# Kernel optimization log

Measured on AMD Instinct MI355X. Metric: run time of the kernel, lower is better.

Reference implementation:

```python
import jax, jax.numpy as jnp
import numpy as np

NUM_GRAPHS = 256
N_NODES = 100000
N_EDGES = 1200000
NODE_DIM = 64
NUM_LAYERS = 3
R_HID = 128
R_OUT = 32


def setup_inputs() -> dict:
    key = jax.random.key(0)
    ks = jax.random.split(key, 10)
    x = jax.random.normal(ks[0], (N_NODES, NODE_DIM), dtype=jnp.float32)
    src = jax.random.randint(ks[1], (N_EDGES,), 0, N_NODES)
    dst = jax.random.randint(ks[2], (N_EDGES,), 0, N_NODES)
    graph_ids = jnp.sort(jax.random.randint(ks[3], (N_NODES,), 0, NUM_GRAPHS))
    s = 1.0 / np.sqrt(NODE_DIM)
    gin_W = jax.random.normal(ks[4], (NUM_LAYERS, NODE_DIM, NODE_DIM), dtype=jnp.float32) * s
    gin_b = jnp.zeros((NUM_LAYERS, NODE_DIM), dtype=jnp.float32)
    eps = jnp.zeros((NUM_LAYERS,), dtype=jnp.float32)  # learnable GIN epsilon
    in_dim = NODE_DIM * NUM_LAYERS
    r_W1 = jax.random.normal(ks[5], (in_dim, R_HID), dtype=jnp.float32) / np.sqrt(in_dim)
    r_b1 = jnp.zeros((R_HID,), dtype=jnp.float32)
    r_W2 = jax.random.normal(ks[6], (R_HID, R_OUT), dtype=jnp.float32) / np.sqrt(R_HID)
    r_b2 = jnp.zeros((R_OUT,), dtype=jnp.float32)
    return {"x": x, "gin_W": gin_W, "gin_b": gin_b, "eps": eps,
            "r_W1": r_W1, "r_b1": r_b1, "r_W2": r_W2, "r_b2": r_b2,
            "src": src, "dst": dst, "graph_ids": graph_ids}


def reference(x, gin_W, gin_b, eps, r_W1, r_b1, r_W2, r_b2, src, dst, graph_ids):
    n = x.shape[0]
    h = x
    hs = []
    for l in range(NUM_LAYERS):  # fixed small layer loop
        # neighbor sum aggregation: scatter-add messages h[src] into dst
        agg = jax.ops.segment_sum(h[src], dst, num_segments=n)  # [N, D]
        h = jax.nn.relu(((1.0 + eps[l]) * h + agg) @ gin_W[l] + gin_b[l])
        hs.append(h)
    H = jnp.stack(hs, axis=1)  # [N, L, D]
    # dgl.sum_nodes per layer output == ragged segment-sum over graph ids
    g = jax.ops.segment_sum(H, graph_ids, num_segments=NUM_GRAPHS)  # [B, L, D]
    g = g.reshape(NUM_GRAPHS, -1)  # [B, L*D]
    # readout MLP (2 layers)
    out = jax.nn.relu(g @ r_W1 + r_b1) @ r_W2 + r_b2
    return out
```

## Files before the change

kernel.cpp:

```cpp
#include <hip/hip_runtime.h>


#define SPLIT 16
#define NBLK 512
#define BS 512

typedef unsigned short ushort_t;
typedef __bf16 v8bf __attribute__((ext_vector_type(8)));
typedef float v4f __attribute__((ext_vector_type(4)));

__device__ __forceinline__ float h2f_lo(unsigned int v) {
    return (float)__builtin_bit_cast(_Float16, (unsigned short)(v & 0xffffu));
}
__device__ __forceinline__ float h2f_hi(unsigned int v) {
    return (float)__builtin_bit_cast(_Float16, (unsigned short)(v >> 16));
}
__device__ __forceinline__ unsigned int f2h(float f) {
    return (unsigned int)__builtin_bit_cast(unsigned short, (_Float16)f);
}

__global__ __launch_bounds__(256) void pre_kernel(
        const int* __restrict__ dst, int* __restrict__ cnt2d,
        int E, int nbkt, int ebpb,
        const float* __restrict__ x, ushort_t* __restrict__ xh, int n4, int castBlocks,
        const float* __restrict__ W, ushort_t* __restrict__ whi,
        ushort_t* __restrict__ wlo, int wtotal) {
    __shared__ int lcnt[256];
    int t = threadIdx.x;
    int blk = blockIdx.x;
    if (blk < NBLK) {
        lcnt[t] = 0;
        __syncthreads();
        int base = blk * ebpb;
        int end = min(base + ebpb, E);
        for (int i = base + t; i < end; i += 256)
            atomicAdd(&lcnt[dst[i] >> 9], 1);
        __syncthreads();
        if (t < nbkt) cnt2d[(size_t)blk * nbkt + t] = lcnt[t];
    } else if (blk < NBLK + castBlocks) {
        int i = (blk - NBLK) * 256 + t;
        if (i < n4) {
            float4 v = ((const float4*)x)[i];
            uint2 p;
            p.x = f2h(v.x) | (f2h(v.y) << 16);
            p.y = f2h(v.z) | (f2h(v.w) << 16);
            ((uint2*)xh)[i] = p;
        }
    } else {
        int i = (blk - NBLK - castBlocks) * 256 + t;
        if (i < wtotal) {
            int l = i >> 12, r = i & 4095;
            int n = r >> 6, k = r & 63;
            float w = W[l * 4096 + k * 64 + n];
            __bf16 h = (__bf16)w;
            float rem = w - (float)h;
            whi[i] = __builtin_bit_cast(ushort_t, h);
            wlo[i] = __builtin_bit_cast(ushort_t, (__bf16)rem);
        }
    }
}

__global__ __launch_bounds__(256) void colscan_kernel(
        const int* __restrict__ cnt2d, int* __restrict__ blkoff,
        int* __restrict__ btot, int nbkt) {
    __shared__ int sh[256];
    int b = blockIdx.x, t = threadIdx.x;
    int i0 = 2 * t, i1 = 2 * t + 1;
    int v0 = cnt2d[(size_t)i0 * nbkt + b];
    int v1 = cnt2d[(size_t)i1 * nbkt + b];
    int pair = v0 + v1;
    sh[t] = pair;
    __syncthreads();
    for (int off = 1; off < 256; off <<= 1) {
        int u = (t >= off) ? sh[t - off] : 0;
        __syncthreads();
        sh[t] += u;
        __syncthreads();
    }
    int ex = sh[t] - pair;
    blkoff[(size_t)b * NBLK + i0] = ex;
    blkoff[(size_t)b * NBLK + i1] = ex + v0;
    if (t == 255) btot[b] = sh[255];
}

__global__ __launch_bounds__(256) void bucket_base_kernel(
        const int* __restrict__ btot, int* __restrict__ bbase,
        int* __restrict__ offsets, int nbkt, int N, int E) {
    __shared__ int sh[256];
    int t = threadIdx.x;
    int v = (t < nbkt) ? btot[t] : 0;
    sh[t] = v;
    __syncthreads();
    for (int off = 1; off < 256; off <<= 1) {
        int u = (t >= off) ? sh[t - off] : 0;
        __syncthreads();
        sh[t] += u;
        __syncthreads();
    }
    if (t < nbkt) bbase[t] = sh[t] - v;
    if (t == 0) { bbase[nbkt] = E; offsets[N] = E; }
}

__global__ __launch_bounds__(256) void bucket_scatter_kernel(
        const int* __restrict__ src, const int* __restrict__ dst,
        const int* __restrict__ bbase, const int* __restrict__ blkoff,
        unsigned int* __restrict__ bkt, int E, int nbkt, int ebpb) {
    __shared__ int lbase[256];
    __shared__ int lrank[256];
    int t = threadIdx.x;
    if (t < nbkt) lbase[t] = bbase[t] + blkoff[(size_t)t * NBLK + blockIdx.x];
    lrank[t] = 0;
    __syncthreads();
    int base = blockIdx.x * ebpb;
    int end = min(base + ebpb, E);
    for (int i = base + t; i < end; i += 256) {
        int d = dst[i];
        int b = d >> 9;
        int r = atomicAdd(&lrank[b], 1);
        bkt[lbase[b] + r] = ((unsigned int)src[i] << 9) | (unsigned int)(d & (BS - 1));
    }
}

__global__ __launch_bounds__(256) void csr_build_kernel(
        const unsigned int* __restrict__ bkt, const int* __restrict__ bbase,
        int* __restrict__ offsets, int* __restrict__ csr, int N, int nbkt) {
    __shared__ int cnt[BS];
    __shared__ int rank[BS];
    __shared__ int sh[256];
    int b = blockIdx.x, t = threadIdx.x;
    cnt[t] = 0; cnt[t + 256] = 0;
    rank[t] = 0; rank[t + 256] = 0;
    __syncthreads();
    int base = bbase[b], end = bbase[b + 1];
    for (int i = base + t; i < end; i += 256)
        atomicAdd(&cnt[bkt[i] & (BS - 1)], 1);
    __syncthreads();
    int i0 = 2 * t, i1 = 2 * t + 1;
    int v0 = cnt[i0], v1 = cnt[i1];
    int pair = v0 + v1;
    sh[t] = pair;
    __syncthreads();
    for (int off = 1; off < 256; off <<= 1) {
        int u = (t >= off) ? sh[t - off] : 0;
        __syncthreads();
        sh[t] += u;
        __syncthreads();
    }
    int ex = sh[t] - pair;
    __syncthreads();
    cnt[i0] = ex;
    cnt[i1] = ex + v0;
    __syncthreads();
    int d0 = (b << 9) + i0;
    if (d0 <= N) offsets[d0] = base + cnt[i0];
    int d1 = (b << 9) + i1;
    if (d1 <= N) offsets[d1] = base + cnt[i1];
    for (int i = base + t; i < end; i += 256) {
        unsigned int v = bkt[i];
        int dl = v & (BS - 1);
        int r = atomicAdd(&rank[dl], 1);
        csr[base + cnt[dl] + r] = (int)(v >> 9);
    }
}

__global__ __launch_bounds__(256) void layer_kernel(
        const ushort_t* __restrict__ hin, ushort_t* __restrict__ hout,
        const int* __restrict__ offsets, const int* __restrict__ csr,
        const ushort_t* __restrict__ wt_hi, const ushort_t* __restrict__ wt_lo,
        const float* __restrict__ gin_b, const float* __restrict__ eps_arr,
        int layer, int N) {
    __shared__ float rows[4 * 16 * 64];
    int t = threadIdx.x;
    int wv = t >> 6, lane = t & 63;
    int tile = blockIdx.x * 4 + wv;
    if (tile * 16 >= N) return;
    float* myrows = rows + wv * 16 * 64;
    float eps1 = 1.0f + eps_arr[layer];

    int g  = lane >> 4;
    int sl = lane & 15;

    int off_l = offsets[min(tile * 16 + lane, N)];

    int e0n = __shfl(off_l, 0, 64);
    int degn = __shfl(off_l, 1, 64) - e0n;
    int idxn = (lane < degn) ? csr[e0n + lane] : 0;

    for (int k = 0; k < 16; ++k) {
        int e0k = e0n, degk = degn, idxk = idxn;
        if (k < 15) {
            e0n = __shfl(off_l, k + 1, 64);
            degn = __shfl(off_l, k + 2, 64) - e0n;
            idxn = (lane < degn) ? csr[e0n + lane] : 0;
        }
        float ax = 0.f, ay = 0.f, az = 0.f, aw = 0.f;
        int dcap = min(degk, 64);
        #pragma unroll 8
        for (int j = g; j < dcap; j += 4) {
            int s = __shfl(idxk, j, 64);
            uint2 v = ((const uint2*)(hin + (size_t)s * 64))[sl];
            ax += h2f_lo(v.x); ay += h2f_hi(v.x);
            az += h2f_lo(v.y); aw += h2f_hi(v.y);
        }
        for (int j = 64 + g; j < degk; j += 4) {
            int s = csr[e0k + j];
            uint2 v = ((const uint2*)(hin + (size_t)s * 64))[sl];
            ax += h2f_lo(v.x); ay += h2f_hi(v.x);
            az += h2f_lo(v.y); aw += h2f_hi(v.y);
        }
        ax += __shfl_xor(ax, 16, 64); ax += __shfl_xor(ax, 32, 64);
        ay += __shfl_xor(ay, 16, 64); ay += __shfl_xor(ay, 32, 64);
        az += __shfl_xor(az, 16, 64); az += __shfl_xor(az, 32, 64);
        aw += __shfl_xor(aw, 16, 64); aw += __shfl_xor(aw, 32, 64);

        int node = tile * 16 + k;
        if (node < N) {
            uint2 self = ((const uint2*)(hin + (size_t)node * 64))[sl];
            ax = fmaf(eps1, h2f_lo(self.x), ax);
            ay = fmaf(eps1, h2f_hi(self.x), ay);
            az = fmaf(eps1, h2f_lo(self.y), az);
            aw = fmaf(eps1, h2f_hi(self.y), aw);
        }
        if (g == 0) {
            float4 r4; r4.x = ax; r4.y = ay; r4.z = az; r4.w = aw;
            *(float4*)&myrows[k * 64 + sl * 4] = r4;
        }
    }

    int c = lane & 15;
    int q = lane >> 4;
    int node16 = tile * 16 + c;

    const ushort_t* Whi = wt_hi + layer * 4096;
    const ushort_t* Wlo = wt_lo + layer * 4096;
    const float*    bl  = gin_b + layer * 64;

    v8bf bhi[2], blo2[2];
    #pragma unroll
    for (int kt = 0; kt < 2; ++kt) {
        float4 f0 = *(float4*)&myrows[c * 64 + kt * 32 + q * 8];
        float4 f1 = *(float4*)&myrows[c * 64 + kt * 32 + q * 8 + 4];
        float xs[8] = {f0.x, f0.y, f0.z, f0.w, f1.x, f1.y, f1.z, f1.w};
        #pragma unroll
        for (int j = 0; j < 8; ++j) {
            __bf16 h = (__bf16)xs[j];
            bhi[kt][j] = h;
            blo2[kt][j] = (__bf16)(xs[j] - (float)h);
        }
    }

    #pragma unroll
    for (int mt = 0; mt < 4; ++mt) {
        v4f acc = {0.f, 0.f, 0.f, 0.f};
        #pragma unroll
        for (int kt = 0; kt < 2; ++kt) {
            int dim = mt * 16 + c;
            size_t off = (size_t)dim * 64 + kt * 32 + q * 8;
            v8bf ah = __builtin_bit_cast(v8bf, *(const uint4*)(Whi + off));
            v8bf al = __builtin_bit_cast(v8bf, *(const uint4*)(Wlo + off));
            acc = __builtin_amdgcn_mfma_f32_16x16x32_bf16(ah, bhi[kt],  acc, 0, 0, 0);
            acc = __builtin_amdgcn_mfma_f32_16x16x32_bf16(ah, blo2[kt], acc, 0, 0, 0);
            acc = __builtin_amdgcn_mfma_f32_16x16x32_bf16(al, bhi[kt],  acc, 0, 0, 0);
        }
        float4 bv = ((const float4*)(bl + mt * 16))[q];
        float o0 = fmaxf(acc[0] + bv.x, 0.f);
        float o1 = fmaxf(acc[1] + bv.y, 0.f);
        float o2 = fmaxf(acc[2] + bv.z, 0.f);
        float o3 = fmaxf(acc[3] + bv.w, 0.f);
        uint2 pk;
        pk.x = f2h(o0) | (f2h(o1) << 16);
        pk.y = f2h(o2) | (f2h(o3) << 16);
        if (node16 < N)
            *(uint2*)(hout + (size_t)node16 * 64 + mt * 16 + q * 4) = pk;
    }
}

__global__ __launch_bounds__(192) void readout_part_kernel(
        const ushort_t* __restrict__ H, const int* __restrict__ gids,
        float* __restrict__ gpart, int N) {
    int graph = blockIdx.x / SPLIT;
    int sp    = blockIdx.x % SPLIT;
    int lo = 0, hi = N;
    while (lo < hi) { int mid = (lo + hi) >> 1; if (gids[mid] < graph) lo = mid + 1; else hi = mid; }
    int start = lo;
    int lo2 = start, hi2 = N;
    while (lo2 < hi2) { int mid = (lo2 + hi2) >> 1; if (gids[mid] < graph + 1) lo2 = mid + 1; else hi2 = mid; }
    int end = lo2;
    int t = threadIdx.x;
    int l = t >> 6, d = t & 63;
    float acc = 0.0f;
    int cnt = end - start;
    if (cnt > 0) {
        int per = (cnt + SPLIT - 1) / SPLIT;
        int cs = start + sp * per;
        int ce = min(cs + per, end);
        const ushort_t* Hl = H + (size_t)l * N * 64;
        for (int n = cs; n < ce; ++n)
            acc += (float)__builtin_bit_cast(_Float16, Hl[(size_t)n * 64 + d]);
    }
    gpart[(size_t)(graph * SPLIT + sp) * 192 + t] = acc;
}

__global__ __launch_bounds__(192) void mlp_kernel(
        const float* __restrict__ gpart,
        const float* __restrict__ W1, const float* __restrict__ b1,
        const float* __restrict__ W2, const float* __restrict__ b2,
        float* __restrict__ out) {
    __shared__ float gr[192];
    __shared__ float hid[128];
    int graph = blockIdx.x;
    int t = threadIdx.x;
    float a = 0.f;
    #pragma unroll
    for (int sp = 0; sp < SPLIT; ++sp)
        a += gpart[(size_t)(graph * SPLIT + sp) * 192 + t];
    gr[t] = a;
    __syncthreads();
    if (t < 128) {
        float s = b1[t];
        for (int k = 0; k < 192; ++k) s = fmaf(gr[k], W1[k * 128 + t], s);
        hid[t] = fmaxf(s, 0.0f);
    }
    __syncthreads();
    if (t < 32) {
        float s = b2[t];
        for (int k = 0; k < 128; ++k) s = fmaf(hid[k], W2[k * 32 + t], s);
        out[graph * 32 + t] = s;
    }
}

extern "C" void kernel_launch(void* const* d_in, const int* in_sizes, int n_in,
                              void* d_out, int out_size, void* d_ws, size_t ws_size,
                              hipStream_t stream) {
    const float* x     = (const float*)d_in[0];
    const float* gin_W = (const float*)d_in[1];
    const float* gin_b = (const float*)d_in[2];
    const float* eps   = (const float*)d_in[3];
    const float* r_W1  = (const float*)d_in[4];
    const float* r_b1  = (const float*)d_in[5];
    const float* r_W2  = (const float*)d_in[6];
    const float* r_b2  = (const float*)d_in[7];
    const int*   src   = (const int*)d_in[8];
    const int*   dst   = (const int*)d_in[9];
    const int*   gids  = (const int*)d_in[10];

    int N = in_sizes[0] / 64;
    int E = in_sizes[8];
    int B = out_size / 32;

    int nbkt = (N + BS - 1) / BS;
    int ebpb = (E + NBLK - 1) / NBLK;
    int n4 = N * 64 / 4;
    int castBlocks = (n4 + 255) / 256;
    int wtotal = 3 * 4096;
    int prepBlocks = (wtotal + 255) / 256;

    int* ws       = (int*)d_ws;
    float* gpart  = (float*)ws;
    int* cnt2d    = ws + (size_t)B * SPLIT * 192;
    int* blkoff   = cnt2d + (size_t)NBLK * nbkt;
    int* btot     = blkoff + (size_t)nbkt * NBLK;
    int* bbase    = btot + nbkt;
    int* offsets  = bbase + (nbkt + 1);
    unsigned int* bkt = (unsigned int*)(offsets + (N + 1));
    int* csr      = (int*)(bkt + E);
    size_t w      = (size_t)(csr + E - ws);
    w = (w + 15) & ~(size_t)15;
    ushort_t* xh  = (ushort_t*)(ws + w);
    ushort_t* H   = xh + (size_t)N * 64;
    ushort_t* whi = H + 3 * (size_t)N * 64;
    ushort_t* wlo = whi + 3 * 4096;

    pre_kernel<<<NBLK + castBlocks + prepBlocks, 256, 0, stream>>>(
        dst, cnt2d, E, nbkt, ebpb, x, xh, n4, castBlocks, gin_W, whi, wlo, wtotal);
    colscan_kernel<<<nbkt, 256, 0, stream>>>(cnt2d, blkoff, btot, nbkt);
    bucket_base_kernel<<<1, 256, 0, stream>>>(btot, bbase, offsets, nbkt, N, E);
    bucket_scatter_kernel<<<NBLK, 256, 0, stream>>>(src, dst, bbase, blkoff, bkt, E, nbkt, ebpb);
    csr_build_kernel<<<nbkt, 256, 0, stream>>>(bkt, bbase, offsets, csr, N, nbkt);

    int lbk = (N + 63) / 64;
    ushort_t* H0 = H;
    ushort_t* H1 = H + (size_t)N * 64;
    ushort_t* H2 = H + 2 * (size_t)N * 64;

    layer_kernel<<<lbk, 256, 0, stream>>>(xh, H0, offsets, csr, whi, wlo, gin_b, eps, 0, N);
    layer_kernel<<<lbk, 256, 0, stream>>>(H0, H1, offsets, csr, whi, wlo, gin_b, eps, 1, N);
    layer_kernel<<<lbk, 256, 0, stream>>>(H1, H2, offsets, csr, whi, wlo, gin_b, eps, 2, N);

    readout_part_kernel<<<B * SPLIT, 192, 0, stream>>>(H, gids, gpart, N);
    mlp_kernel<<<B, 192, 0, stream>>>(gpart, r_W1, r_b1, r_W2, r_b2, (float*)d_out);
}
```

Measured before the change: 315.4 us.

## Software-pipeline neighbor row gathers across nodes with double-buffered register prefetch

Restructures the GIN aggregation loop so gathered neighbor rows for the next node (up to 6 per lane group) are issued into a register buffer before the current node is reduced. CSR index loads are prefetched three nodes ahead and offsets are broadcast via readfirstlane. Blocks shrink to 128 threads with launch bounds for higher occupancy. The aim is to hide gather latency; the cost is higher register pressure and more complex control flow.

```diff
diff --git a/kernel.cpp b/kernel.cpp
--- a/kernel.cpp
+++ b/kernel.cpp
@@ -4,6 +4,7 @@
 #define SPLIT 16
 #define NBLK 512
 #define BS 512
+#define PF 6
 
 typedef unsigned short ushort_t;
 typedef __bf16 v8bf __attribute__((ext_vector_type(8)));
@@ -17,6 +18,9 @@
 }
 __device__ __forceinline__ unsigned int f2h(float f) {
     return (unsigned int)__builtin_bit_cast(unsigned short, (_Float16)f);
+}
+__device__ __forceinline__ int rdl_shfl(int v, int srcLane) {
+    return __builtin_amdgcn_readfirstlane(__shfl(v, srcLane, 64));
 }
 
 __global__ __launch_bounds__(256) void pre_kernel(
@@ -163,16 +167,80 @@
     }
 }
 
-__global__ __launch_bounds__(256) void layer_kernel(
+struct RowBuf {
+    uint2 r0, r1, r2, r3, r4, r5;
+    uint2 sf;
+};
+
+__device__ __forceinline__ void issue_rows(RowBuf& b, const ushort_t* __restrict__ hin,
+        int idxv, int dg, int node, int N, int g, int sl) {
+    int trip = min((dg + 3) >> 2, PF);
+#define ISSUE_SLOT(nn, rr)                                         \
+    if (nn < trip) {                                               \
+        int p = g + 4 * nn;                                        \
+        int s = __shfl(idxv, p, 64);                               \
+        uint2 v = make_uint2(0u, 0u);                              \
+        if (p < dg) v = ((const uint2*)hin)[s * 16 + sl];          \
+        b.rr = v;                                                  \
+    }
+    ISSUE_SLOT(0, r0) ISSUE_SLOT(1, r1) ISSUE_SLOT(2, r2)
+    ISSUE_SLOT(3, r3) ISSUE_SLOT(4, r4) ISSUE_SLOT(5, r5)
+#undef ISSUE_SLOT
+    b.sf = make_uint2(0u, 0u);
+    if (node < N) b.sf = ((const uint2*)hin)[node * 16 + sl];
+}
+
+__device__ __forceinline__ void consume_node(const RowBuf& b, const ushort_t* __restrict__ hin,
+        const int* __restrict__ csr, int idxv, int e0, int dg,
+        int g, int sl, float eps1, float* myrows, int k) {
+    int trip = min((dg + 3) >> 2, PF);
+    float ax = 0.f, ay = 0.f, az = 0.f, aw = 0.f;
+#define ACC(vv) { ax += h2f_lo(vv.x); ay += h2f_hi(vv.x);          \
+                  az += h2f_lo(vv.y); aw += h2f_hi(vv.y); }
+    if (0 < trip) ACC(b.r0)
+    if (1 < trip) ACC(b.r1)
+    if (2 < trip) ACC(b.r2)
+    if (3 < trip) ACC(b.r3)
+    if (4 < trip) ACC(b.r4)
+    if (5 < trip) ACC(b.r5)
+    if (dg > 4 * PF) {
+        int dcap = min(dg, 64);
+        for (int j = 4 * PF + g; j < dcap; j += 4) {
+            int s = __shfl(idxv, j, 64);
+            uint2 v = ((const uint2*)hin)[s * 16 + sl];
+            ACC(v)
+        }
+        for (int j = 64 + g; j < dg; j += 4) {
+            int s = csr[e0 + j];
+            uint2 v = ((const uint2*)hin)[s * 16 + sl];
+            ACC(v)
+        }
+    }
+#undef ACC
+    ax += __shfl_xor(ax, 16, 64); ax += __shfl_xor(ax, 32, 64);
+    ay += __shfl_xor(ay, 16, 64); ay += __shfl_xor(ay, 32, 64);
+    az += __shfl_xor(az, 16, 64); az += __shfl_xor(az, 32, 64);
+    aw += __shfl_xor(aw, 16, 64); aw += __shfl_xor(aw, 32, 64);
+    ax = fmaf(eps1, h2f_lo(b.sf.x), ax);
+    ay = fmaf(eps1, h2f_hi(b.sf.x), ay);
+    az = fmaf(eps1, h2f_lo(b.sf.y), az);
+    aw = fmaf(eps1, h2f_hi(b.sf.y), aw);
+    if (g == 0) {
+        float4 r4; r4.x = ax; r4.y = ay; r4.z = az; r4.w = aw;
+        *(float4*)&myrows[k * 64 + sl * 4] = r4;
+    }
+}
+
+__global__ __launch_bounds__(128, 8) void layer_kernel(
         const ushort_t* __restrict__ hin, ushort_t* __restrict__ hout,
         const int* __restrict__ offsets, const int* __restrict__ csr,
         const ushort_t* __restrict__ wt_hi, const ushort_t* __restrict__ wt_lo,
         const float* __restrict__ gin_b, const float* __restrict__ eps_arr,
         int layer, int N) {
-    __shared__ float rows[4 * 16 * 64];
+    __shared__ float rows[2 * 16 * 64];
     int t = threadIdx.x;
     int wv = t >> 6, lane = t & 63;
-    int tile = blockIdx.x * 4 + wv;
+    int tile = blockIdx.x * 2 + wv;
     if (tile * 16 >= N) return;
     float* myrows = rows + wv * 16 * 64;
     float eps1 = 1.0f + eps_arr[layer];
@@ -182,50 +250,32 @@
 
     int off_l = offsets[min(tile * 16 + lane, N)];
 
-    int e0n = __shfl(off_l, 0, 64);
-    int degn = __shfl(off_l, 1, 64) - e0n;
-    int idxn = (lane < degn) ? csr[e0n + lane] : 0;
-
-    for (int k = 0; k < 16; ++k) {
-        int e0k = e0n, degk = degn, idxk = idxn;
-        if (k < 15) {
-            e0n = __shfl(off_l, k + 1, 64);
-            degn = __shfl(off_l, k + 2, 64) - e0n;
-            idxn = (lane < degn) ? csr[e0n + lane] : 0;
-        }
-        float ax = 0.f, ay = 0.f, az = 0.f, aw = 0.f;
-        int dcap = min(degk, 64);
-        #pragma unroll 8
-        for (int j = g; j < dcap; j += 4) {
-            int s = __shfl(idxk, j, 64);
-            uint2 v = ((const uint2*)(hin + (size_t)s * 64))[sl];
-            ax += h2f_lo(v.x); ay += h2f_hi(v.x);
-            az += h2f_lo(v.y); aw += h2f_hi(v.y);
-        }
-        for (int j = 64 + g; j < degk; j += 4) {
-            int s = csr[e0k + j];
-            uint2 v = ((const uint2*)(hin + (size_t)s * 64))[sl];
-            ax += h2f_lo(v.x); ay += h2f_hi(v.x);
-            az += h2f_lo(v.y); aw += h2f_hi(v.y);
-        }
-        ax += __shfl_xor(ax, 16, 64); ax += __shfl_xor(ax, 32, 64);
-        ay += __shfl_xor(ay, 16, 64); ay += __shfl_xor(ay, 32, 64);
-        az += __shfl_xor(az, 16, 64); az += __shfl_xor(az, 32, 64);
-        aw += __shfl_xor(aw, 16, 64); aw += __shfl_xor(aw, 32, 64);
-
-        int node = tile * 16 + k;
-        if (node < N) {
-            uint2 self = ((const uint2*)(hin + (size_t)node * 64))[sl];
-            ax = fmaf(eps1, h2f_lo(self.x), ax);
-            ay = fmaf(eps1, h2f_hi(self.x), ay);
-            az = fmaf(eps1, h2f_lo(self.y), az);
-            aw = fmaf(eps1, h2f_hi(self.y), aw);
-        }
-        if (g == 0) {
-            float4 r4; r4.x = ax; r4.y = ay; r4.z = az; r4.w = aw;
-            *(float4*)&myrows[k * 64 + sl * 4] = r4;
-        }
-    }
+#define EDEG(kk, e0v, dgv) { e0v = rdl_shfl(off_l, kk); \
+                             dgv = rdl_shfl(off_l, (kk) + 1) - e0v; }
+
+    int e0P, dgP, e0Q, dgQ, e0R, dgR;
+    EDEG(0, e0P, dgP); EDEG(1, e0Q, dgQ); EDEG(2, e0R, dgR);
+    int idxP = (lane < dgP) ? csr[e0P + lane] : 0;
+    int idxQ = (lane < dgQ) ? csr[e0Q + lane] : 0;
+    int idxR = (lane < dgR) ? csr[e0R + lane] : 0;
+    RowBuf bufA, bufB;
+    issue_rows(bufA, hin, idxP, dgP, tile * 16, N, g, sl);
+
+    for (int kk = 0; kk < 8; ++kk) {
+        int k = kk << 1;
+        int e0S = 0, dgS = 0, idxS = 0;
+        if (k + 3 < 16) { EDEG(k + 3, e0S, dgS); idxS = (lane < dgS) ? csr[e0S + lane] : 0; }
+        issue_rows(bufB, hin, idxQ, dgQ, tile * 16 + k + 1, N, g, sl);
+        consume_node(bufA, hin, csr, idxP, e0P, dgP, g, sl, eps1, myrows, k);
+        int e0T = 0, dgT = 0, idxT = 0;
+        if (k + 4 < 16) { EDEG(k + 4, e0T, dgT); idxT = (lane < dgT) ? csr[e0T + lane] : 0; }
+        if (k + 2 < 16) issue_rows(bufA, hin, idxR, dgR, tile * 16 + k + 2, N, g, sl);
+        consume_node(bufB, hin, csr, idxQ, e0Q, dgQ, g, sl, eps1, myrows, k + 1);
+        idxP = idxR; e0P = e0R; dgP = dgR;
+        idxQ = idxS; e0Q = e0S; dgQ = dgS;
+        idxR = idxT; e0R = e0T; dgR = dgT;
+    }
+#undef EDEG
 
     int c = lane & 15;
     int q = lane >> 4;
@@ -378,14 +428,14 @@
     bucket_scatter_kernel<<<NBLK, 256, 0, stream>>>(src, dst, bbase, blkoff, bkt, E, nbkt, ebpb);
     csr_build_kernel<<<nbkt, 256, 0, stream>>>(bkt, bbase, offsets, csr, N, nbkt);
 
-    int lbk = (N + 63) / 64;
+    int lbk = (N + 31) / 32;
     ushort_t* H0 = H;
     ushort_t* H1 = H + (size_t)N * 64;
     ushort_t* H2 = H + 2 * (size_t)N * 64;
 
-    layer_kernel<<<lbk, 256, 0, stream>>>(xh, H0, offsets, csr, whi, wlo, gin_b, eps, 0, N);
-    layer_kernel<<<lbk, 256, 0, stream>>>(H0, H1, offsets, csr, whi, wlo, gin_b, eps, 1, N);
-    layer_kernel<<<lbk, 256, 0, stream>>>(H1, H2, offsets, csr, whi, wlo, gin_b, eps, 2, N);
+    layer_kernel<<<lbk, 128, 0, stream>>>(xh, H0, offsets, csr, whi, wlo, gin_b, eps, 0, N);
+    layer_kernel<<<lbk, 128, 0, stream>>>(H0, H1, offsets, csr, whi, wlo, gin_b, eps, 1, N);
+    layer_kernel<<<lbk, 128, 0, stream>>>(H1, H2, offsets, csr, whi, wlo, gin_b, eps, 2, N);
 
     readout_part_kernel<<<B * SPLIT, 192, 0, stream>>>(H, gids, gpart, N);
     mlp_kernel<<<B, 192, 0, stream>>>(gpart, r_W1, r_b1, r_W2, r_b2, (float*)d_out);
```

Measured after the change: 319.4 us. No clear change (+1.3%).

## Batch neighbor gathers two nodes at a time to raise memory-level parallelism

Applied to the files above, without the earlier changes.

Restructures the GIN aggregation loop. All 16 nodes' CSR index rows are preloaded up front, then neighbor rows are gathered for two nodes at once, with up to 24 fixed slots per node issued before any accumulation, and self rows are loaded early. A sched_barrier keeps the loads ahead of the consuming adds. This targets gather latency stalls, since average degree is about 12. The cost is higher register pressure, addressed with launch_bounds(256,4), and some wasted loads of row 0 when degree is low.

```diff
diff --git a/kernel.cpp b/kernel.cpp
--- a/kernel.cpp
+++ b/kernel.cpp
@@ -163,73 +163,96 @@
     }
 }
 
-__global__ __launch_bounds__(256) void layer_kernel(
+#define CONSUME_NODE(kk, dgv, e0v, buf, sf) { \
+    float ax = 0.f, ay = 0.f, az = 0.f, aw = 0.f; \
+    _Pragma("unroll") \
+    for (int j = 0; j < 6; ++j) { \
+        if (g + 4 * j < (dgv)) { \
+            ax += h2f_lo(buf[j].x); ay += h2f_hi(buf[j].x); \
+            az += h2f_lo(buf[j].y); aw += h2f_hi(buf[j].y); } } \
+    if ((dgv) > 24) {                    \
+        int dc_ = min((dgv), 64); \
+        for (int j = 24 + g; j < dc_; j += 4) { \
+            int s_ = __shfl(idxa[kk], j, 64); \
+            uint2 v_ = hp2[(size_t)s_ * 16 + sl]; \
+            ax += h2f_lo(v_.x); ay += h2f_hi(v_.x); \
+            az += h2f_lo(v_.y); aw += h2f_hi(v_.y); } \
+        for (int j = 64 + g; j < (dgv); j += 4) {    \
+            int s_ = csr[(e0v) + j]; \
+            uint2 v_ = hp2[(size_t)s_ * 16 + sl]; \
+            ax += h2f_lo(v_.x); ay += h2f_hi(v_.x); \
+            az += h2f_lo(v_.y); aw += h2f_hi(v_.y); } } \
+    ax += __shfl_xor(ax, 16, 64); ax += __shfl_xor(ax, 32, 64); \
+    ay += __shfl_xor(ay, 16, 64); ay += __shfl_xor(ay, 32, 64); \
+    az += __shfl_xor(az, 16, 64); az += __shfl_xor(az, 32, 64); \
+    aw += __shfl_xor(aw, 16, 64); aw += __shfl_xor(aw, 32, 64); \
+    if (tile * 16 + (kk) < N) { \
+        ax = fmaf(eps1, h2f_lo(sf.x), ax); ay = fmaf(eps1, h2f_hi(sf.x), ay); \
+        az = fmaf(eps1, h2f_lo(sf.y), az); aw = fmaf(eps1, h2f_hi(sf.y), aw); } \
+    if (g == 0) { \
+        float4 r4_; r4_.x = ax; r4_.y = ay; r4_.z = az; r4_.w = aw; \
+        *(float4*)&myrows[(kk) * 64 + sl * 4] = r4_; } }
+
+__global__ __launch_bounds__(256, 4) void layer_kernel(
         const ushort_t* __restrict__ hin, ushort_t* __restrict__ hout,
         const int* __restrict__ offsets, const int* __restrict__ csr,
         const ushort_t* __restrict__ wt_hi, const ushort_t* __restrict__ wt_lo,
         const float* __restrict__ gin_b, const float* __restrict__ eps_arr,
-        int layer, int N) {
+        int layer, int N, int E) {
     __shared__ float rows[4 * 16 * 64];
     int t = threadIdx.x;
     int wv = t >> 6, lane = t & 63;
     int tile = blockIdx.x * 4 + wv;
     if (tile * 16 >= N) return;
     float* myrows = rows + wv * 16 * 64;
+    const uint2* hp2 = (const uint2*)hin;
     float eps1 = 1.0f + eps_arr[layer];
 
     int g  = lane >> 4;
     int sl = lane & 15;
 
     int off_l = offsets[min(tile * 16 + lane, N)];
-
-    int e0n = __shfl(off_l, 0, 64);
-    int degn = __shfl(off_l, 1, 64) - e0n;
-    int idxn = (lane < degn) ? csr[e0n + lane] : 0;
-
+    int e0a[17];
+    #pragma unroll
+    for (int k = 0; k < 17; ++k)
+        e0a[k] = __builtin_amdgcn_readlane(off_l, k);
+
+    int idxa[16];
+    #pragma unroll
     for (int k = 0; k < 16; ++k) {
-        int e0k = e0n, degk = degn, idxk = idxn;
-        if (k < 15) {
-            e0n = __shfl(off_l, k + 1, 64);
-            degn = __shfl(off_l, k + 2, 64) - e0n;
-            idxn = (lane < degn) ? csr[e0n + lane] : 0;
-        }
-        float ax = 0.f, ay = 0.f, az = 0.f, aw = 0.f;
-        int dcap = min(degk, 64);
-        #pragma unroll 8
-        for (int j = g; j < dcap; j += 4) {
-            int s = __shfl(idxk, j, 64);
-            uint2 v = ((const uint2*)(hin + (size_t)s * 64))[sl];
-            ax += h2f_lo(v.x); ay += h2f_hi(v.x);
-            az += h2f_lo(v.y); aw += h2f_hi(v.y);
-        }
-        for (int j = 64 + g; j < degk; j += 4) {
-            int s = csr[e0k + j];
-            uint2 v = ((const uint2*)(hin + (size_t)s * 64))[sl];
-            ax += h2f_lo(v.x); ay += h2f_hi(v.x);
-            az += h2f_lo(v.y); aw += h2f_hi(v.y);
-        }
-        ax += __shfl_xor(ax, 16, 64); ax += __shfl_xor(ax, 32, 64);
-        ay += __shfl_xor(ay, 16, 64); ay += __shfl_xor(ay, 32, 64);
-        az += __shfl_xor(az, 16, 64); az += __shfl_xor(az, 32, 64);
-        aw += __shfl_xor(aw, 16, 64); aw += __shfl_xor(aw, 32, 64);
-
-        int node = tile * 16 + k;
-        if (node < N) {
-            uint2 self = ((const uint2*)(hin + (size_t)node * 64))[sl];
-            ax = fmaf(eps1, h2f_lo(self.x), ax);
-            ay = fmaf(eps1, h2f_hi(self.x), ay);
-            az = fmaf(eps1, h2f_lo(self.y), az);
-            aw = fmaf(eps1, h2f_hi(self.y), aw);
-        }
-        if (g == 0) {
-            float4 r4; r4.x = ax; r4.y = ay; r4.z = az; r4.w = aw;
-            *(float4*)&myrows[k * 64 + sl * 4] = r4;
-        }
-    }
-
-    int c = lane & 15;
-    int q = lane >> 4;
-    int node16 = tile * 16 + c;
+        int dg_ = e0a[k + 1] - e0a[k];
+        int v_ = csr[min(e0a[k] + lane, E - 1)];
+        idxa[k] = (lane < dg_) ? v_ : 0;
+    }
+
+    #pragma unroll
+    for (int kb = 0; kb < 8; ++kb) {
+        const int k = kb * 2;
+        int e0A = e0a[k],     dgA = e0a[k + 1] - e0a[k];
+        int e0B = e0a[k + 1], dgB = e0a[k + 2] - e0a[k + 1];
+        uint2 b[6], c[6];
+        #pragma unroll
+        for (int j = 0; j < 6; ++j) {
+            int p = g + 4 * j;
+            int s = (p < dgA) ? __shfl(idxa[k], p, 64) : 0;
+            b[j] = hp2[(size_t)s * 16 + sl];
+        }
+        #pragma unroll
+        for (int j = 0; j < 6; ++j) {
+            int p = g + 4 * j;
+            int s = (p < dgB) ? __shfl(idxa[k + 1], p, 64) : 0;
+            c[j] = hp2[(size_t)s * 16 + sl];
+        }
+        uint2 sfA = hp2[(size_t)min(tile * 16 + k,     N - 1) * 16 + sl];
+        uint2 sfB = hp2[(size_t)min(tile * 16 + k + 1, N - 1) * 16 + sl];
+        __builtin_amdgcn_sched_barrier(0);
+        CONSUME_NODE(k,     dgA, e0A, b, sfA)
+        CONSUME_NODE(k + 1, dgB, e0B, c, sfB)
+    }
+
+    int c2 = lane & 15;
+    int q  = lane >> 4;
+    int node16 = tile * 16 + c2;
 
     const ushort_t* Whi = wt_hi + layer * 4096;
     const ushort_t* Wlo = wt_lo + layer * 4096;
@@ -238,8 +261,8 @@
     v8bf bhi[2], blo2[2];
     #pragma unroll
     for (int kt = 0; kt < 2; ++kt) {
-        float4 f0 = *(float4*)&myrows[c * 64 + kt * 32 + q * 8];
-        float4 f1 = *(float4*)&myrows[c * 64 + kt * 32 + q * 8 + 4];
+        float4 f0 = *(float4*)&myrows[c2 * 64 + kt * 32 + q * 8];
+        float4 f1 = *(float4*)&myrows[c2 * 64 + kt * 32 + q * 8 + 4];
         float xs[8] = {f0.x, f0.y, f0.z, f0.w, f1.x, f1.y, f1.z, f1.w};
         #pragma unroll
         for (int j = 0; j < 8; ++j) {
@@ -254,7 +277,7 @@
         v4f acc = {0.f, 0.f, 0.f, 0.f};
         #pragma unroll
         for (int kt = 0; kt < 2; ++kt) {
-            int dim = mt * 16 + c;
+            int dim = mt * 16 + c2;
             size_t off = (size_t)dim * 64 + kt * 32 + q * 8;
             v8bf ah = __builtin_bit_cast(v8bf, *(const uint4*)(Whi + off));
             v8bf al = __builtin_bit_cast(v8bf, *(const uint4*)(Wlo + off));
@@ -383,9 +406,9 @@
     ushort_t* H1 = H + (size_t)N * 64;
     ushort_t* H2 = H + 2 * (size_t)N * 64;
 
-    layer_kernel<<<lbk, 256, 0, stream>>>(xh, H0, offsets, csr, whi, wlo, gin_b, eps, 0, N);
-    layer_kernel<<<lbk, 256, 0, stream>>>(H0, H1, offsets, csr, whi, wlo, gin_b, eps, 1, N);
-    layer_kernel<<<lbk, 256, 0, stream>>>(H1, H2, offsets, csr, whi, wlo, gin_b, eps, 2, N);
+    layer_kernel<<<lbk, 256, 0, stream>>>(xh, H0, offsets, csr, whi, wlo, gin_b, eps, 0, N, E);
+    layer_kernel<<<lbk, 256, 0, stream>>>(H0, H1, offsets, csr, whi, wlo, gin_b, eps, 1, N, E);
+    layer_kernel<<<lbk, 256, 0, stream>>>(H1, H2, offsets, csr, whi, wlo, gin_b, eps, 2, N, E);
 
     readout_part_kernel<<<B * SPLIT, 192, 0, stream>>>(H, gids, gpart, N);
     mlp_kernel<<<B, 192, 0, stream>>>(gpart, r_W1, r_b1, r_W2, r_b2, (float*)d_out);
```

Measured after the change: 307.3 us. 1.03x faster.

## Share one 16-node tile across four waves in the GIN layer kernel

Applied to the files above, without the earlier changes.

Each block now handles a single 16-node tile instead of four. Each wave gathers neighbors for 4 of the 16 nodes, the rows go to shared memory behind a block barrier, and each wave computes one 16-column slice of the MFMA output. This cuts per-wave serial gather length and MFMA work and shrinks shared memory, with launch bounds raised to allow more resident blocks. It adds a __syncthreads, launches four times as many blocks, and makes each block read the CSR offsets redundantly.

```diff
diff --git a/kernel.cpp b/kernel.cpp
--- a/kernel.cpp
+++ b/kernel.cpp
@@ -163,18 +163,18 @@
     }
 }
 
-__global__ __launch_bounds__(256) void layer_kernel(
+__global__ __launch_bounds__(256, 8) void layer_kernel(
         const ushort_t* __restrict__ hin, ushort_t* __restrict__ hout,
         const int* __restrict__ offsets, const int* __restrict__ csr,
         const ushort_t* __restrict__ wt_hi, const ushort_t* __restrict__ wt_lo,
         const float* __restrict__ gin_b, const float* __restrict__ eps_arr,
         int layer, int N) {
-    __shared__ float rows[4 * 16 * 64];
+    __shared__ float rows[16 * 64];
     int t = threadIdx.x;
     int wv = t >> 6, lane = t & 63;
-    int tile = blockIdx.x * 4 + wv;
+    int tile = blockIdx.x;
     if (tile * 16 >= N) return;
-    float* myrows = rows + wv * 16 * 64;
+    const uint2* hp2 = (const uint2*)hin;
     float eps1 = 1.0f + eps_arr[layer];
 
     int g  = lane >> 4;
@@ -182,15 +182,17 @@
 
     int off_l = offsets[min(tile * 16 + lane, N)];
 
-    int e0n = __shfl(off_l, 0, 64);
-    int degn = __shfl(off_l, 1, 64) - e0n;
+    int kb = wv * 4;
+    int e0n = __shfl(off_l, kb, 64);
+    int degn = __shfl(off_l, kb + 1, 64) - e0n;
     int idxn = (lane < degn) ? csr[e0n + lane] : 0;
 
-    for (int k = 0; k < 16; ++k) {
+    for (int k2 = 0; k2 < 4; ++k2) {
+        int kk = kb + k2;
         int e0k = e0n, degk = degn, idxk = idxn;
-        if (k < 15) {
-            e0n = __shfl(off_l, k + 1, 64);
-            degn = __shfl(off_l, k + 2, 64) - e0n;
+        if (k2 < 3) {
+            e0n = __shfl(off_l, kk + 1, 64);
+            degn = __shfl(off_l, kk + 2, 64) - e0n;
             idxn = (lane < degn) ? csr[e0n + lane] : 0;
         }
         float ax = 0.f, ay = 0.f, az = 0.f, aw = 0.f;
@@ -198,13 +200,13 @@
         #pragma unroll 8
         for (int j = g; j < dcap; j += 4) {
             int s = __shfl(idxk, j, 64);
-            uint2 v = ((const uint2*)(hin + (size_t)s * 64))[sl];
+            uint2 v = hp2[(size_t)s * 16 + sl];
             ax += h2f_lo(v.x); ay += h2f_hi(v.x);
             az += h2f_lo(v.y); aw += h2f_hi(v.y);
         }
         for (int j = 64 + g; j < degk; j += 4) {
             int s = csr[e0k + j];
-            uint2 v = ((const uint2*)(hin + (size_t)s * 64))[sl];
+            uint2 v = hp2[(size_t)s * 16 + sl];
             ax += h2f_lo(v.x); ay += h2f_hi(v.x);
             az += h2f_lo(v.y); aw += h2f_hi(v.y);
         }
@@ -213,9 +215,9 @@
         az += __shfl_xor(az, 16, 64); az += __shfl_xor(az, 32, 64);
         aw += __shfl_xor(aw, 16, 64); aw += __shfl_xor(aw, 32, 64);
 
-        int node = tile * 16 + k;
+        int node = tile * 16 + kk;
         if (node < N) {
-            uint2 self = ((const uint2*)(hin + (size_t)node * 64))[sl];
+            uint2 self = hp2[(size_t)node * 16 + sl];
             ax = fmaf(eps1, h2f_lo(self.x), ax);
             ay = fmaf(eps1, h2f_hi(self.x), ay);
             az = fmaf(eps1, h2f_lo(self.y), az);
@@ -223,13 +225,15 @@
         }
         if (g == 0) {
             float4 r4; r4.x = ax; r4.y = ay; r4.z = az; r4.w = aw;
-            *(float4*)&myrows[k * 64 + sl * 4] = r4;
-        }
-    }
-
-    int c = lane & 15;
-    int q = lane >> 4;
-    int node16 = tile * 16 + c;
+            *(float4*)&rows[kk * 64 + sl * 4] = r4;
+        }
+    }
+    __syncthreads();
+
+    int c2 = lane & 15;
+    int q  = lane >> 4;
+    int node16 = tile * 16 + c2;
+    int mt = wv;
 
     const ushort_t* Whi = wt_hi + layer * 4096;
     const ushort_t* Wlo = wt_lo + layer * 4096;
@@ -238,8 +242,8 @@
     v8bf bhi[2], blo2[2];
     #pragma unroll
     for (int kt = 0; kt < 2; ++kt) {
-        float4 f0 = *(float4*)&myrows[c * 64 + kt * 32 + q * 8];
-        float4 f1 = *(float4*)&myrows[c * 64 + kt * 32 + q * 8 + 4];
+        float4 f0 = *(float4*)&rows[c2 * 64 + kt * 32 + q * 8];
+        float4 f1 = *(float4*)&rows[c2 * 64 + kt * 32 + q * 8 + 4];
         float xs[8] = {f0.x, f0.y, f0.z, f0.w, f1.x, f1.y, f1.z, f1.w};
         #pragma unroll
         for (int j = 0; j < 8; ++j) {
@@ -249,30 +253,27 @@
         }
     }
 
+    v4f acc = {0.f, 0.f, 0.f, 0.f};
     #pragma unroll
-    for (int mt = 0; mt < 4; ++mt) {
-        v4f acc = {0.f, 0.f, 0.f, 0.f};
-        #pragma unroll
-        for (int kt = 0; kt < 2; ++kt) {
-            int dim = mt * 16 + c;
-            size_t off = (size_t)dim * 64 + kt * 32 + q * 8;
-            v8bf ah = __builtin_bit_cast(v8bf, *(const uint4*)(Whi + off));
-            v8bf al = __builtin_bit_cast(v8bf, *(const uint4*)(Wlo + off));
-            acc = __builtin_amdgcn_mfma_f32_16x16x32_bf16(ah, bhi[kt],  acc, 0, 0, 0);
-            acc = __builtin_amdgcn_mfma_f32_16x16x32_bf16(ah, blo2[kt], acc, 0, 0, 0);
-            acc = __builtin_amdgcn_mfma_f32_16x16x32_bf16(al, bhi[kt],  acc, 0, 0, 0);
-        }
-        float4 bv = ((const float4*)(bl + mt * 16))[q];
-        float o0 = fmaxf(acc[0] + bv.x, 0.f);
-        float o1 = fmaxf(acc[1] + bv.y, 0.f);
-        float o2 = fmaxf(acc[2] + bv.z, 0.f);
-        float o3 = fmaxf(acc[3] + bv.w, 0.f);
-        uint2 pk;
-        pk.x = f2h(o0) | (f2h(o1) << 16);
-        pk.y = f2h(o2) | (f2h(o3) << 16);
-        if (node16 < N)
-            *(uint2*)(hout + (size_t)node16 * 64 + mt * 16 + q * 4) = pk;
-    }
+    for (int kt = 0; kt < 2; ++kt) {
+        int dim = mt * 16 + c2;
+        size_t off = (size_t)dim * 64 + kt * 32 + q * 8;
+        v8bf ah = __builtin_bit_cast(v8bf, *(const uint4*)(Whi + off));
+        v8bf al = __builtin_bit_cast(v8bf, *(const uint4*)(Wlo + off));
+        acc = __builtin_amdgcn_mfma_f32_16x16x32_bf16(ah, bhi[kt],  acc, 0, 0, 0);
+        acc = __builtin_amdgcn_mfma_f32_16x16x32_bf16(ah, blo2[kt], acc, 0, 0, 0);
+        acc = __builtin_amdgcn_mfma_f32_16x16x32_bf16(al, bhi[kt],  acc, 0, 0, 0);
+    }
+    float4 bv = ((const float4*)(bl + mt * 16))[q];
+    float o0 = fmaxf(acc[0] + bv.x, 0.f);
+    float o1 = fmaxf(acc[1] + bv.y, 0.f);
+    float o2 = fmaxf(acc[2] + bv.z, 0.f);
+    float o3 = fmaxf(acc[3] + bv.w, 0.f);
+    uint2 pk;
+    pk.x = f2h(o0) | (f2h(o1) << 16);
+    pk.y = f2h(o2) | (f2h(o3) << 16);
+    if (node16 < N)
+        *(uint2*)(hout + (size_t)node16 * 64 + mt * 16 + q * 4) = pk;
 }
 
 __global__ __launch_bounds__(192) void readout_part_kernel(
@@ -378,7 +379,7 @@
     bucket_scatter_kernel<<<NBLK, 256, 0, stream>>>(src, dst, bbase, blkoff, bkt, E, nbkt, ebpb);
     csr_build_kernel<<<nbkt, 256, 0, stream>>>(bkt, bbase, offsets, csr, N, nbkt);
 
-    int lbk = (N + 63) / 64;
+    int lbk = (N + 15) / 16;
     ushort_t* H0 = H;
     ushort_t* H1 = H + (size_t)N * 64;
     ushort_t* H2 = H + 2 * (size_t)N * 64;
```

Result: slower. 330.9 us (+4.9%).
